# Optimization experiments

Hardware: AMD Instinct MI355X
Metric: run time of the kernel (lower is better)

## Reference

```python
import jax, jax.numpy as jnp
import numpy as np
from jax import lax

B, C_IN, C_OUT, K, STYLE_DIM, H, W = 8, 512, 512, 3, 512, 64, 64


def setup_inputs() -> dict:
    key = jax.random.key(0)
    k1, k2, k3, k4 = jax.random.split(key, 4)
    return {
        "x": jax.random.normal(k1, (B, C_IN, H, W), dtype=jnp.float32),
        "style": jax.random.normal(k2, (B, STYLE_DIM), dtype=jnp.float32),
        "w": jax.random.normal(k3, (1, C_OUT, C_IN, K, K), dtype=jnp.float32),
        "affine_w": jax.random.normal(k4, (C_IN, STYLE_DIM), dtype=jnp.float32),
        "affine_b": jnp.ones((C_IN,), dtype=jnp.float32),  # bias_init=1
    }


def _per_sample_conv(xi, wi):
    # xi: [C_in, H, W], wi: [C_out, C_in, K, K]; 'same' padding, stride 1
    p = K // 2
    out = lax.conv_general_dilated(
        xi[None], wi, window_strides=(1, 1), padding=[(p, p), (p, p)],
        dimension_numbers=("NCHW", "OIHW", "NCHW"))
    return out[0]


def reference(x, style, w, affine_w, affine_b):
    # Affine (FullyConnected_Layer, linear act, lr_multiplier=1)
    weight_gain_fc = 1.0 / np.sqrt(STYLE_DIM)
    s = style @ (affine_w * weight_gain_fc).T + affine_b  # [B, C_in]

    # Modulate
    weight_gain = 1.0 / np.sqrt(C_IN * K * K)
    weight = w * weight_gain * s[:, None, :, None, None]  # [B, C_out, C_in, K, K]

    # Demodulate
    decoefs = lax.rsqrt(jnp.sum(weight * weight, axis=(2, 3, 4)) + 1e-8)  # [B, C_out]
    weight = weight * decoefs[:, :, None, None, None]

    # Per-sample conv (equivalent to groups=B grouped conv2d)
    out = jax.vmap(_per_sample_conv)(x, weight)  # [B, C_out, H, W]
    return out
```

## Files before the change

### kernel.cpp

```cpp
#include <hip/hip_runtime.h>
#include <hip/hip_bf16.h>


#define CDIM 512
#define HW 64
#define CK 32
#define NCHUNK 16

typedef __attribute__((ext_vector_type(8))) short short8;
typedef __attribute__((ext_vector_type(4))) float float4v;

__device__ __forceinline__ short f2bf(float f) {
    unsigned u = __float_as_uint(f);
    unsigned r = (u + 0x7FFFu + ((u >> 16) & 1u)) >> 16;
    return (short)r;
}

__device__ __forceinline__ void async_ld16(const short* g, short* l) {
    __builtin_amdgcn_global_load_lds(
        (const __attribute__((address_space(1))) void*)g,
        (__attribute__((address_space(3))) void*)l, 16, 0, 0);
}

__device__ __forceinline__ void hard_sync() {
    asm volatile("s_waitcnt vmcnt(0) lgkmcnt(0)" ::: "memory");
    __builtin_amdgcn_sched_barrier(0);
    __builtin_amdgcn_s_barrier();
    __builtin_amdgcn_sched_barrier(0);
}


__global__ void k_affine(const float* __restrict__ style, const float* __restrict__ aw,
                         const float* __restrict__ ab, float* __restrict__ s) {
    int gid = blockIdx.x * 4 + (threadIdx.x >> 6);
    int lane = threadIdx.x & 63;
    int b = gid >> 9, ci = gid & 511;
    const float4v* st = (const float4v*)(style + b * CDIM);
    const float4v* wp = (const float4v*)(aw + ci * CDIM);
    float acc = 0.f;
#pragma unroll
    for (int k = 0; k < 2; ++k) {
        float4v a = st[lane * 2 + k], w = wp[lane * 2 + k];
        acc += a[0] * w[0] + a[1] * w[1] + a[2] * w[2] + a[3] * w[3];
    }
#pragma unroll
    for (int off = 32; off; off >>= 1) acc += __shfl_down(acc, off);
    if (lane == 0) s[gid] = acc * 0.04419417382415922f + ab[ci];
}

__global__ void k_ws2(const float* __restrict__ w, float* __restrict__ ws2) {
    int i = blockIdx.x * 256 + threadIdx.x;
    const float* p = w + i * 9;
    float a = 0.f;
#pragma unroll
    for (int t = 0; t < 9; ++t) a += p[t] * p[t];
    ws2[i] = a;
}

__global__ void k_oscale(const float* __restrict__ s, const float* __restrict__ ws2,
                         float* __restrict__ osc) {
    int gid = blockIdx.x * 4 + (threadIdx.x >> 6);
    int lane = threadIdx.x & 63;
    int b = gid >> 9, co = gid & 511;
    const float4v* sp = (const float4v*)(s + b * CDIM);
    const float4v* rp = (const float4v*)(ws2 + co * CDIM);
    float acc = 0.f;
#pragma unroll
    for (int k = 0; k < 2; ++k) {
        float4v a = sp[lane * 2 + k], r = rp[lane * 2 + k];
        acc += a[0] * a[0] * r[0] + a[1] * a[1] * r[1]
             + a[2] * a[2] * r[2] + a[3] * a[3] * r[3];
    }
#pragma unroll
    for (int off = 32; off; off >>= 1) acc += __shfl_down(acc, off);
    const float wg = 0.014731391274719739f;
    const float wg2 = 2.170138888888889e-4f;
    if (lane == 0) osc[gid] = wg * rsqrtf(wg2 * acc + 1e-8f);
}

__global__ void k_wconv(const float* __restrict__ w, short* __restrict__ wgt) {
    int idx = blockIdx.x * 256 + threadIdx.x;
    int j = idx & 7;
    int slotg = idx >> 3;
    int region = slotg / 4608;
    int a16 = slotg - region * 4608;
    int tm = a16 >> 6;
    int t = tm >> 3;
    int mf = tm & 7;
    int sl = a16 & 63;
    int l4 = sl >> 4;
    int l15 = sl & 15;
    int ct = region & 3;
    int c = region >> 2;
    int co = ct * 128 + mf * 16 + l15;
    int ci = c * 32 + l4 * 8 + j;
    wgt[idx] = f2bf(w[(co * CDIM + ci) * 9 + t]);
}

__global__ void k_xs(const float* __restrict__ x, const float* __restrict__ s,
                     short* __restrict__ xs) {
    const int bx = blockIdx.x;
    const int grow = bx & 63;
    const int t = bx >> 6;
    const int c = t & 15;
    const int b = t >> 4;
    const int q = threadIdx.x >> 6;
    const int lane = threadIdx.x & 63;
    const int cig = q ^ (((lane + 1) >> 1) & 3);
    const int ci0 = c * 32 + cig * 8;
    const float* xb = x + ((b * CDIM + ci0) * HW + grow) * HW + lane;
    const float* sb = s + b * CDIM + ci0;
    short8 pk;
#pragma unroll
    for (int j = 0; j < 8; ++j)
        pk[j] = f2bf(xb[j * (HW * HW)] * sb[j]);
    *(short8*)&xs[bx * 2048 + lane * 32 + q * 8] = pk;
}

__global__ __launch_bounds__(1024, 1) void conv_main2(
    const short* __restrict__ xs, const short* __restrict__ zs,
    const short* __restrict__ wgt, const float* __restrict__ osc,
    float* __restrict__ out) {

    __shared__ __align__(16) short w_lds[9 * 8 * 64 * 8];
    __shared__ __align__(16) short x_lds[2][10 * 66 * CK];

    const int tid = threadIdx.x;
    const int lane = tid & 63;
    const int wid = tid >> 6;
    const int wr = wid >> 1;
    const int wm = wid & 1;
    const int l15 = lane & 15;
    const int l4 = lane >> 4;

    const int bx = blockIdx.x;
    const int xcd = bx & 7;
    const int t7 = bx >> 3;
    const int ct = t7 & 3;
    const int ghi = t7 >> 2;
    const int b = xcd;
    const int r0 = ghi * 8;

    if (tid < 640) {
        int bufi = tid >= 320;
        int v = tid - bufi * 320;
        int row = v >> 5;
        int w16 = v & 31;
        int colh = (w16 >= 16) ? 65 : 0;
        int q16 = w16 & 15;
        ((unsigned*)x_lds[bufi])[(row * 66 + colh) * 16 + q16] = 0u;
    }

    auto stage_w = [&](int c) {
        const short* src = wgt + (c * 4 + ct) * 36864;
#pragma unroll
        for (int k = 0; k < 5; ++k) {
            int u = tid + 1024 * k;
            if (u >= 4608) u -= 4608;
            async_ld16(src + u * 8, w_lds + u * 8);
        }
    };

    auto stage_x = [&](int c, int buf) {
        const short* xsb = xs + ((b * 16 + c) << 17);
#pragma unroll
        for (int k = 0; k < 3; ++k) {
            int u = wid + 16 * k;
            if (u >= 40) u -= 40;
            int row = u >> 2;
            int part = u & 3;
            int grow = r0 - 1 + row;
            const short* src = (grow >= 0 && grow < HW)
                ? xsb + grow * 2048 + part * 512
                : zs + part * 512;
            short* dst = &x_lds[buf][(row * 66 + 1) * CK] + part * 512;
            async_ld16(src + lane * 8, dst + lane * 8);
        }
    };

    float4v acc[4][4] = {};

    auto compute = [&](int buf) {
        const short* xb = x_lds[buf];
#pragma unroll
        for (int t = 0; t < 9; ++t) {
            int dh = t / 3 - 1;
            int dw = t % 3 - 1;
            int lrow = wr + dh + 1;
            short8 bfr[4];
#pragma unroll
            for (int nf = 0; nf < 4; ++nf) {
                int lcol = 1 + nf * 16 + l15 + dw;
                int xq = l4 ^ ((lcol >> 1) & 3);
                bfr[nf] = *(const short8*)&xb[(lrow * 66 + lcol) * CK + xq * 8];
            }
#pragma unroll
            for (int mf = 0; mf < 4; ++mf) {
                short8 af = *(const short8*)&w_lds[((t * 8 + wm * 4 + mf) * 64 + lane) * 8];
#pragma unroll
                for (int nf = 0; nf < 4; ++nf)
                    acc[mf][nf] = __builtin_amdgcn_mfma_f32_16x16x32_bf16(
                        af, bfr[nf], acc[mf][nf], 0, 0, 0);
            }
        }
    };

    stage_w(0);
    stage_x(0, 0);
    stage_x(1, 1);
    __builtin_amdgcn_sched_barrier(0);
    asm volatile("s_waitcnt vmcnt(3) lgkmcnt(0)" ::: "memory");
    __builtin_amdgcn_sched_barrier(0);
    __builtin_amdgcn_s_barrier();
    __builtin_amdgcn_sched_barrier(0);

    int cur = 0;
#pragma unroll 1
    for (int c = 0; c < NCHUNK; ++c) {
        __builtin_amdgcn_s_setprio(1);
        compute(cur);
        __builtin_amdgcn_s_setprio(0);

        __builtin_amdgcn_sched_barrier(0);
        asm volatile("s_waitcnt lgkmcnt(0)" ::: "memory");
        __builtin_amdgcn_s_barrier();
        __builtin_amdgcn_sched_barrier(0);

        const int cc1 = (c + 1 < NCHUNK) ? c + 1 : NCHUNK - 1;
        const int cc2 = (c + 2 < NCHUNK) ? c + 2 : NCHUNK - 1;
        stage_w(cc1);
        stage_x(cc2, cur);
        __builtin_amdgcn_sched_barrier(0);

        asm volatile("s_waitcnt vmcnt(3)" ::: "memory");
        __builtin_amdgcn_sched_barrier(0);
        __builtin_amdgcn_s_barrier();
        __builtin_amdgcn_sched_barrier(0);
        cur ^= 1;
    }

    asm volatile("s_waitcnt vmcnt(0)" ::: "memory");

    const int row_out = r0 + wr;
#pragma unroll
    for (int mf = 0; mf < 4; ++mf) {
        float4v ov = *(const float4v*)&osc[b * CDIM + ct * 128 + (wm * 4 + mf) * 16 + l4 * 4];
#pragma unroll
        for (int j = 0; j < 4; ++j) {
            int co = ct * 128 + (wm * 4 + mf) * 16 + l4 * 4 + j;
            float* po = out + ((b * CDIM + co) * HW + row_out) * HW;
#pragma unroll
            for (int nf = 0; nf < 4; ++nf)
                po[nf * 16 + l15] = acc[mf][nf][j] * ov[j];
        }
    }
}

__global__ __launch_bounds__(512, 1) void conv_main_fb(
    const float* __restrict__ x, const float* __restrict__ s,
    const short* __restrict__ wgt, const float* __restrict__ osc,
    float* __restrict__ out) {

    __shared__ __align__(16) short w_lds[9 * 8 * 64 * 8];
    __shared__ __align__(16) short x_lds[2][10 * 66 * CK];

    const int tid = threadIdx.x;
    const int lane = tid & 63;
    const int wid = tid >> 6;
    const int l15 = lane & 15;
    const int l4 = lane >> 4;

    const int bx = blockIdx.x;
    const int xcd = bx & 7;
    const int t7 = bx >> 3;
    const int ct = t7 & 3;
    const int ghi = t7 >> 2;
    const int b = xcd;
    const int r0 = ghi * 8;

    const int cig = tid & 3;
    const int col = (tid >> 2) & 63;
    const int rowhalf = tid >> 8;

    for (int i = tid; i < 640; i += 512) {
        int bufi = i >= 320;
        int v = i - bufi * 320;
        int row = v >> 5;
        int w16 = v & 31;
        int colh = (w16 >= 16) ? 65 : 0;
        int q16 = w16 & 15;
        ((unsigned*)x_lds[bufi])[(row * 66 + colh) * 16 + q16] = 0u;
    }

    float rx[40];
    float4v sva, svb;

    auto stage_w = [&](int c) {
        const short* src = wgt + (c * 4 + ct) * 36864;
#pragma unroll
        for (int k = 0; k < 9; ++k) {
            int off = (k * 512 + wid * 64) * 8;
            async_ld16(src + off + lane * 8, w_lds + off);
        }
    };

    auto stage_x_load = [&](int c) {
        const float4v* sp = (const float4v*)&s[b * CDIM + c * 32 + cig * 8];
        sva = sp[0]; svb = sp[1];
#pragma unroll
        for (int i = 0; i < 5; ++i) {
            int row = 2 * i + rowhalf;
            int grow = r0 - 1 + row;
            bool ok = (grow >= 0) && (grow < HW);
            const float* base = x + ((b * CDIM + c * 32 + cig * 8) * HW + (ok ? grow : 0)) * HW + col;
#pragma unroll
            for (int j = 0; j < 8; ++j) {
                float v = base[j * (HW * HW)];
                rx[i * 8 + j] = ok ? v : 0.0f;
            }
        }
    };

    auto stage_x_write = [&](int buf) {
        int lcol = col + 1;
        int q = cig ^ ((lcol >> 1) & 3);
#pragma unroll
        for (int i = 0; i < 5; ++i) {
            int row = 2 * i + rowhalf;
            short8 pk;
#pragma unroll
            for (int j = 0; j < 8; ++j) {
                float sj = (j < 4) ? sva[j] : svb[j - 4];
                pk[j] = f2bf(rx[i * 8 + j] * sj);
            }
            *(short8*)&x_lds[buf][(row * 66 + lcol) * CK + q * 8] = pk;
        }
    };

    float4v acc[8][4] = {};

    auto compute = [&](int buf) {
        const short* xb = x_lds[buf];
#pragma unroll
        for (int t = 0; t < 9; ++t) {
            int dh = t / 3 - 1;
            int dw = t % 3 - 1;
            int lrow = wid + dh + 1;
            short8 bfr[4];
#pragma unroll
            for (int nf = 0; nf < 4; ++nf) {
                int lcol = 1 + nf * 16 + l15 + dw;
                int xq = l4 ^ ((lcol >> 1) & 3);
                bfr[nf] = *(const short8*)&xb[(lrow * 66 + lcol) * CK + xq * 8];
            }
#pragma unroll
            for (int mf = 0; mf < 8; ++mf) {
                short8 af = *(const short8*)&w_lds[((t * 8 + mf) * 64 + lane) * 8];
#pragma unroll
                for (int nf = 0; nf < 4; ++nf)
                    acc[mf][nf] = __builtin_amdgcn_mfma_f32_16x16x32_bf16(
                        af, bfr[nf], acc[mf][nf], 0, 0, 0);
            }
        }
    };

    stage_w(0);
    stage_x_load(0);
    stage_x_write(0);
    hard_sync();

    int cur = 0;
#pragma unroll 1
    for (int c = 0; c < NCHUNK; ++c) {
        if (c + 1 < NCHUNK) stage_x_load(c + 1);
        compute(cur);
        if (c + 1 < NCHUNK) {
            hard_sync();
            stage_w(c + 1);
            stage_x_write(cur ^ 1);
            hard_sync();
            cur ^= 1;
        }
    }

    const int row_out = r0 + wid;
#pragma unroll
    for (int mf = 0; mf < 8; ++mf) {
        float4v ov = *(const float4v*)&osc[b * CDIM + ct * 128 + mf * 16 + l4 * 4];
#pragma unroll
        for (int j = 0; j < 4; ++j) {
            int co = ct * 128 + mf * 16 + l4 * 4 + j;
            float* po = out + ((b * CDIM + co) * HW + row_out) * HW;
#pragma unroll
            for (int nf = 0; nf < 4; ++nf)
                po[nf * 16 + l15] = acc[mf][nf][j] * ov[j];
        }
    }
}


extern "C" void kernel_launch(void* const* d_in, const int* in_sizes, int n_in,
                              void* d_out, int out_size, void* d_ws, size_t ws_size,
                              hipStream_t stream) {
    const float* x     = (const float*)d_in[0];
    const float* style = (const float*)d_in[1];
    const float* w     = (const float*)d_in[2];
    const float* aw    = (const float*)d_in[3];
    const float* ab    = (const float*)d_in[4];
    float* out = (float*)d_out;

    char* wsb = (char*)d_ws;
    float* s_buf = (float*)(wsb);
    float* ws2   = (float*)(wsb + 16384);
    float* osc   = (float*)(wsb + 1064960);
    short* wgt   = (short*)(wsb + 1081344);
    short* zs    = (short*)(wsb + 5799936);
    short* xs    = (short*)(wsb + 5804032);
    const size_t need = 5804032ull + 33554432ull;

    k_affine<<<1024, 256, 0, stream>>>(style, aw, ab, s_buf);
    k_ws2<<<1024, 256, 0, stream>>>(w, ws2);
    k_wconv<<<9216, 256, 0, stream>>>(w, wgt);
    k_oscale<<<1024, 256, 0, stream>>>(s_buf, ws2, osc);

    if (ws_size >= need) {
        hipMemsetAsync(zs, 0, 4096, stream);
        k_xs<<<8192, 256, 0, stream>>>(x, s_buf, xs);
        conv_main2<<<256, 1024, 0, stream>>>(xs, zs, wgt, osc, out);
    } else {
        conv_main_fb<<<256, 512, 0, stream>>>(x, s_buf, wgt, osc, out);
    }
}
```

Baseline: 180.3 us.

## Read activations directly from global memory and double-buffer weights in LDS

```diff
diff --git a/kernel.cpp b/kernel.cpp
--- a/kernel.cpp
+++ b/kernel.cpp
@@ -4,8 +4,8 @@
 
 #define CDIM 512
 #define HW 64
-#define CK 32
 #define NCHUNK 16
+#define XROW 2112
 
 typedef __attribute__((ext_vector_type(8))) short short8;
 typedef __attribute__((ext_vector_type(4))) float float4v;
@@ -104,32 +104,35 @@
     const int t = bx >> 6;
     const int c = t & 15;
     const int b = t >> 4;
-    const int q = threadIdx.x >> 6;
-    const int lane = threadIdx.x & 63;
-    const int cig = q ^ (((lane + 1) >> 1) & 3);
-    const int ci0 = c * 32 + cig * 8;
-    const float* xb = x + ((b * CDIM + ci0) * HW + grow) * HW + lane;
+    const int px = threadIdx.x >> 2;
+    const int sl = threadIdx.x & 3;
+    const int ci0 = c * 32 + sl * 8;
+    const float* xb = x + ((b * CDIM + ci0) * HW + grow) * HW + px;
     const float* sb = s + b * CDIM + ci0;
     short8 pk;
 #pragma unroll
     for (int j = 0; j < 8; ++j)
         pk[j] = f2bf(xb[j * (HW * HW)] * sb[j]);
-    *(short8*)&xs[bx * 2048 + lane * 32 + q * 8] = pk;
-}
-
-__global__ __launch_bounds__(1024, 1) void conv_main2(
-    const short* __restrict__ xs, const short* __restrict__ zs,
+    short* rowp = xs + (size_t)bx * XROW;
+    *(short8*)&rowp[(px + 1) * 32 + sl * 8] = pk;
+    if (threadIdx.x < 8) {
+        int col = (threadIdx.x >> 2) ? 65 : 0;
+        int s2 = threadIdx.x & 3;
+        short8 z = {};
+        *(short8*)&rowp[col * 32 + s2 * 8] = z;
+    }
+}
+
+__global__ __launch_bounds__(512, 1) void conv_main3(
+    const short* __restrict__ xs, const short* __restrict__ zrow,
     const short* __restrict__ wgt, const float* __restrict__ osc,
     float* __restrict__ out) {
 
-    __shared__ __align__(16) short w_lds[9 * 8 * 64 * 8];
-    __shared__ __align__(16) short x_lds[2][10 * 66 * CK];
+    __shared__ __align__(16) short w_lds[2][36864];
 
     const int tid = threadIdx.x;
     const int lane = tid & 63;
-    const int wid = tid >> 6;
-    const int wr = wid >> 1;
-    const int wm = wid & 1;
+    const int wr = tid >> 6;
     const int l15 = lane & 15;
     const int l4 = lane >> 4;
 
@@ -141,113 +144,70 @@
     const int b = xcd;
     const int r0 = ghi * 8;
 
-    if (tid < 640) {
-        int bufi = tid >= 320;
-        int v = tid - bufi * 320;
-        int row = v >> 5;
-        int w16 = v & 31;
-        int colh = (w16 >= 16) ? 65 : 0;
-        int q16 = w16 & 15;
-        ((unsigned*)x_lds[bufi])[(row * 66 + colh) * 16 + q16] = 0u;
-    }
-
-    auto stage_w = [&](int c) {
+    const int voff = l15 * 32 + l4 * 8;
+
+    auto stage_w = [&](int c, int bufn) {
         const short* src = wgt + (c * 4 + ct) * 36864;
-#pragma unroll
-        for (int k = 0; k < 5; ++k) {
-            int u = tid + 1024 * k;
-            if (u >= 4608) u -= 4608;
-            async_ld16(src + u * 8, w_lds + u * 8);
-        }
-    };
-
-    auto stage_x = [&](int c, int buf) {
-        const short* xsb = xs + ((b * 16 + c) << 17);
-#pragma unroll
-        for (int k = 0; k < 3; ++k) {
-            int u = wid + 16 * k;
-            if (u >= 40) u -= 40;
-            int row = u >> 2;
-            int part = u & 3;
-            int grow = r0 - 1 + row;
-            const short* src = (grow >= 0 && grow < HW)
-                ? xsb + grow * 2048 + part * 512
-                : zs + part * 512;
-            short* dst = &x_lds[buf][(row * 66 + 1) * CK] + part * 512;
-            async_ld16(src + lane * 8, dst + lane * 8);
-        }
-    };
-
-    float4v acc[4][4] = {};
-
-    auto compute = [&](int buf) {
-        const short* xb = x_lds[buf];
-#pragma unroll
-        for (int t = 0; t < 9; ++t) {
-            int dh = t / 3 - 1;
-            int dw = t % 3 - 1;
-            int lrow = wr + dh + 1;
-            short8 bfr[4];
-#pragma unroll
-            for (int nf = 0; nf < 4; ++nf) {
-                int lcol = 1 + nf * 16 + l15 + dw;
-                int xq = l4 ^ ((lcol >> 1) & 3);
-                bfr[nf] = *(const short8*)&xb[(lrow * 66 + lcol) * CK + xq * 8];
-            }
-#pragma unroll
-            for (int mf = 0; mf < 4; ++mf) {
-                short8 af = *(const short8*)&w_lds[((t * 8 + wm * 4 + mf) * 64 + lane) * 8];
-#pragma unroll
-                for (int nf = 0; nf < 4; ++nf)
-                    acc[mf][nf] = __builtin_amdgcn_mfma_f32_16x16x32_bf16(
-                        af, bfr[nf], acc[mf][nf], 0, 0, 0);
-            }
-        }
-    };
-
-    stage_w(0);
-    stage_x(0, 0);
-    stage_x(1, 1);
-    __builtin_amdgcn_sched_barrier(0);
-    asm volatile("s_waitcnt vmcnt(3) lgkmcnt(0)" ::: "memory");
-    __builtin_amdgcn_sched_barrier(0);
-    __builtin_amdgcn_s_barrier();
-    __builtin_amdgcn_sched_barrier(0);
-
-    int cur = 0;
+        short* dstb = &w_lds[bufn][0];
+#pragma unroll
+        for (int k = 0; k < 9; ++k) {
+            int off = (k * 512 + wr * 64) * 8;
+            async_ld16(src + off + lane * 8, dstb + off + lane * 8);
+        }
+    };
+
+    float4v acc[8][4] = {};
+
+#define TAPX(T)                                                                  \
+    { const short* pd = ((T) < 3) ? p0 : (((T) < 6) ? p1 : p2);                  \
+      const int dwp1 = (T) % 3;                                 \
+      short8 bfr[4];                                                             \
+      _Pragma("unroll")                                                          \
+      for (int nf = 0; nf < 4; ++nf)                                             \
+          bfr[nf] = *(const short8*)(pd + voff + (nf * 16 + dwp1) * 32);         \
+      _Pragma("unroll")                                                          \
+      for (int mf = 0; mf < 8; ++mf) {                                           \
+          short8 af = *(const short8*)&wb[(((T) * 8 + mf) * 64 + lane) * 8];     \
+          _Pragma("unroll")                                                      \
+          for (int nf = 0; nf < 4; ++nf)                                         \
+              acc[mf][nf] = __builtin_amdgcn_mfma_f32_16x16x32_bf16(             \
+                  af, bfr[nf], acc[mf][nf], 0, 0, 0);                            \
+      } }
+
+    stage_w(0, 0);
+    hard_sync();
+
+    const int gb = r0 + wr - 1;
 #pragma unroll 1
     for (int c = 0; c < NCHUNK; ++c) {
+        const int buf = c & 1;
+        const short* wb = &w_lds[buf][0];
+        const short* xcb = xs + ((size_t)(b * 16 + c) * 64) * XROW;
+        const short* p0 = ((unsigned)(gb + 0) < 64u) ? xcb + (size_t)(gb + 0) * XROW : zrow;
+        const short* p1 = ((unsigned)(gb + 1) < 64u) ? xcb + (size_t)(gb + 1) * XROW : zrow;
+        const short* p2 = ((unsigned)(gb + 2) < 64u) ? xcb + (size_t)(gb + 2) * XROW : zrow;
+
+        TAPX(0)
+        stage_w((c + 1 < NCHUNK) ? c + 1 : NCHUNK - 1, buf ^ 1);
         __builtin_amdgcn_s_setprio(1);
-        compute(cur);
+        TAPX(1) TAPX(2) TAPX(3) TAPX(4)
+        TAPX(5) TAPX(6) TAPX(7) TAPX(8)
         __builtin_amdgcn_s_setprio(0);
 
-        __builtin_amdgcn_sched_barrier(0);
-        asm volatile("s_waitcnt lgkmcnt(0)" ::: "memory");
-        __builtin_amdgcn_s_barrier();
-        __builtin_amdgcn_sched_barrier(0);
-
-        const int cc1 = (c + 1 < NCHUNK) ? c + 1 : NCHUNK - 1;
-        const int cc2 = (c + 2 < NCHUNK) ? c + 2 : NCHUNK - 1;
-        stage_w(cc1);
-        stage_x(cc2, cur);
-        __builtin_amdgcn_sched_barrier(0);
-
-        asm volatile("s_waitcnt vmcnt(3)" ::: "memory");
+        asm volatile("s_waitcnt vmcnt(0)" ::: "memory");
         __builtin_amdgcn_sched_barrier(0);
         __builtin_amdgcn_s_barrier();
         __builtin_amdgcn_sched_barrier(0);
-        cur ^= 1;
-    }
-
-    asm volatile("s_waitcnt vmcnt(0)" ::: "memory");
+    }
+#undef TAPX
 
     const int row_out = r0 + wr;
 #pragma unroll
-    for (int mf = 0; mf < 4; ++mf) {
-        float4v ov = *(const float4v*)&osc[b * CDIM + ct * 128 + (wm * 4 + mf) * 16 + l4 * 4];
+    for (int mf = 0; mf < 8; ++mf) {
+        float4v ov = *(const float4v*)&osc[b * CDIM + ct * 128 + mf * 16 + l4 * 4];
 #pragma unroll
         for (int j = 0; j < 4; ++j) {
-            int co = ct * 128 + (wm * 4 + mf) * 16 + l4 * 4 + j;
+            int co = ct * 128 + mf * 16 + l4 * 4 + j;
             float* po = out + ((b * CDIM + co) * HW + row_out) * HW;
 #pragma unroll
             for (int nf = 0; nf < 4; ++nf)
@@ -262,7 +222,7 @@
     float* __restrict__ out) {
 
     __shared__ __align__(16) short w_lds[9 * 8 * 64 * 8];
-    __shared__ __align__(16) short x_lds[2][10 * 66 * CK];
+    __shared__ __align__(16) short x_lds[2][10 * 66 * 32];
 
     const int tid = threadIdx.x;
     const int lane = tid & 63;
@@ -333,7 +293,7 @@
                 float sj = (j < 4) ? sva[j] : svb[j - 4];
                 pk[j] = f2bf(rx[i * 8 + j] * sj);
             }
-            *(short8*)&x_lds[buf][(row * 66 + lcol) * CK + q * 8] = pk;
+            *(short8*)&x_lds[buf][(row * 66 + lcol) * 32 + q * 8] = pk;
         }
     };
 
@@ -351,7 +311,7 @@
             for (int nf = 0; nf < 4; ++nf) {
                 int lcol = 1 + nf * 16 + l15 + dw;
                 int xq = l4 ^ ((lcol >> 1) & 3);
-                bfr[nf] = *(const short8*)&xb[(lrow * 66 + lcol) * CK + xq * 8];
+                bfr[nf] = *(const short8*)&xb[(lrow * 66 + lcol) * 32 + xq * 8];
             }
 #pragma unroll
             for (int mf = 0; mf < 8; ++mf) {
@@ -414,9 +374,9 @@
     float* ws2   = (float*)(wsb + 16384);
     float* osc   = (float*)(wsb + 1064960);
     short* wgt   = (short*)(wsb + 1081344);
-    short* zs    = (short*)(wsb + 5799936);
-    short* xs    = (short*)(wsb + 5804032);
-    const size_t need = 5804032ull + 33554432ull;
+    short* zrow  = (short*)(wsb + 5799936);
+    short* xs    = (short*)(wsb + 5804288);
+    const size_t need = 5804288ull + 34603008ull;
 
     k_affine<<<1024, 256, 0, stream>>>(style, aw, ab, s_buf);
     k_ws2<<<1024, 256, 0, stream>>>(w, ws2);
@@ -424,9 +384,9 @@
     k_oscale<<<1024, 256, 0, stream>>>(s_buf, ws2, osc);
 
     if (ws_size >= need) {
-        hipMemsetAsync(zs, 0, 4096, stream);
+        hipMemsetAsync(zrow, 0, 4352, stream);
         k_xs<<<8192, 256, 0, stream>>>(x, s_buf, xs);
-        conv_main2<<<256, 1024, 0, stream>>>(xs, zs, wgt, osc, out);
+        conv_main3<<<256, 512, 0, stream>>>(xs, zrow, wgt, osc, out);
     } else {
         conv_main_fb<<<256, 512, 0, stream>>>(x, s_buf, wgt, osc, out);
     }
```

Result: faster. 157.5 us (-12.6%).
